# Optimization experiments

Measured on AMD Instinct MI355X. Metric: run time of the kernel, lower is better.

The kernel has to match this reference:

```python
import jax, jax.numpy as jnp
import numpy as np


def sign_fn(x):
    # torch.sign(torch.sign(x) + 0.5): maps x >= 0 -> +1, x < 0 -> -1 (zero -> +1)
    return jnp.where(x >= 0, 1.0, -1.0).astype(x.dtype)


def setup_inputs() -> dict:
    key = jax.random.key(0)
    kx, kw, kb = jax.random.split(key, 3)
    TOKENS, IN, OUT = 8192, 4096, 4096
    x = jax.random.normal(kx, (TOKENS, IN), dtype=jnp.float32)
    weight = jax.random.normal(kw, (OUT, IN), dtype=jnp.float32)
    bias = jax.random.normal(kb, (OUT,), dtype=jnp.float32)
    return {"x": x, "weight": weight, "bias": bias}


def reference(x, weight, bias):
    b_weight = sign_fn(weight)  # [out, in], values in {+1, -1}
    b_bias = sign_fn(bias)      # [out]
    # nn.functional.linear: y = x @ W^T + b
    return jnp.einsum('ti,oi->to', x, b_weight) + b_bias
```

## Files before the change

### kernel.cpp

```cpp
#include <hip/hip_runtime.h>


typedef __attribute__((ext_vector_type(4))) int   i32x4;
typedef __attribute__((ext_vector_type(8))) short short8;
typedef __attribute__((ext_vector_type(4))) float f32x4;

constexpr int M = 8192;
constexpr int N = 4096;
constexpr int K = 4096;

constexpr int BM = 256, BN = 256, BK = 64;
constexpr int NTILES = K / BK;
constexpr int TILE_A = BM * BK;
constexpr int TILE_B = BN * BK;
constexpr int BUFSZ  = TILE_A + TILE_B;
constexpr int RING   = 4;

__device__ __forceinline__ void load_lds16(const void* g, void* l) {
    __builtin_amdgcn_global_load_lds(
        (const __attribute__((address_space(1))) unsigned int*)g,
        (__attribute__((address_space(3))) unsigned int*)l, 16, 0, 0);
}

constexpr int XB = M / 4;
constexpr int WB = 1024;
constexpr int WCH = N * K / 8;

__global__ __launch_bounds__(256) void prep_fused(
    const float* __restrict__ X, const float* __restrict__ W,
    signed char* __restrict__ Xq, signed char* __restrict__ Wq,
    float* __restrict__ Scale) {
    const int t    = threadIdx.x;
    const int lane = t & 63;
    const int wv   = t >> 6;

    if (blockIdx.x < XB) {
        const int row = blockIdx.x * 4 + wv;
        const float4* xr = reinterpret_cast<const float4*>(X + (size_t)row * K);
        float4 v[16];
        float mx = 0.f;
#pragma unroll
        for (int i = 0; i < 4; ++i) {
#pragma unroll
            for (int j = 0; j < 4; ++j) {
                float4 f = xr[4 * lane + 256 * i + j];
                v[4 * i + j] = f;
                mx = fmaxf(mx, fmaxf(fmaxf(fabsf(f.x), fabsf(f.y)),
                                     fmaxf(fabsf(f.z), fabsf(f.w))));
            }
        }
#pragma unroll
        for (int off = 32; off > 0; off >>= 1)
            mx = fmaxf(mx, __shfl_down(mx, off));
        mx = __shfl(mx, 0);
        const float rmax = fmaxf(mx, 1e-20f);
        const float inv  = 127.f / rmax;
        if (lane == 0) Scale[row] = rmax * (1.f / 127.f);

        uint4* out4 = reinterpret_cast<uint4*>(Xq + (size_t)row * K);
#pragma unroll
        for (int i = 0; i < 4; ++i) {
            uint4 o;
            unsigned int* op = &o.x;
#pragma unroll
            for (int j = 0; j < 4; ++j) {
                float4 f = v[4 * i + j];
                int q0 = (int)rintf(f.x * inv);
                int q1 = (int)rintf(f.y * inv);
                int q2 = (int)rintf(f.z * inv);
                int q3 = (int)rintf(f.w * inv);
                op[j] = (q0 & 255) | ((q1 & 255) << 8) |
                        ((q2 & 255) << 16) | ((unsigned)(q3 & 255) << 24);
            }
            out4[lane + 64 * i] = o;
        }
    } else {
        const float4* W4 = reinterpret_cast<const float4*>(W);
        uint2* O = reinterpret_cast<uint2*>(Wq);
        auto sg = [](float f) -> unsigned int { return (f >= 0.f) ? 1u : 0xFFu; };
        size_t idx = (size_t)(blockIdx.x - XB) * 256 + t;
        const size_t stride = (size_t)WB * 256;
        for (size_t c = idx; c < (size_t)WCH; c += stride) {
            float4 a = W4[c * 2], b = W4[c * 2 + 1];
            uint2 o;
            o.x = sg(a.x) | (sg(a.y) << 8) | (sg(a.z) << 16) | (sg(a.w) << 24);
            o.y = sg(b.x) | (sg(b.y) << 8) | (sg(b.z) << 16) | (sg(b.w) << 24);
            O[c] = o;
        }
    }
}

struct GemmCtx {
    const signed char* gA0;
    const signed char* gA1;
    const signed char* gB0;
    const signed char* gB1;
    signed char* lbase;
    int wm, wn, rl, cq16;
};

template <bool STAGE, int VMEND>
__device__ __forceinline__ void kstep2(
    const GemmCtx& c, const signed char* smem, int t,
    i32x4 (&b)[4], i32x4 (&acc)[8][4]) {
    const signed char* Ab = smem + (t & (RING - 1)) * BUFSZ;
    const signed char* Bb = Ab + TILE_A;
    signed char* dst = c.lbase + ((t + 3) & (RING - 1)) * BUFSZ;
    const size_t ko = (size_t)(t + 3) * BK;

    if constexpr (VMEND >= 0)
        asm volatile("s_waitcnt vmcnt(%0)" :: "i"(VMEND) : "memory");
    __builtin_amdgcn_s_barrier();

    i32x4 a0[4];
#pragma unroll
    for (int ni = 0; ni < 4; ++ni)
        b[ni] = *reinterpret_cast<const i32x4*>(
            Bb + (c.wn * 64 + ni * 16 + c.rl) * BK + c.cq16);
#pragma unroll
    for (int mi = 0; mi < 4; ++mi)
        a0[mi] = *reinterpret_cast<const i32x4*>(
            Ab + (c.wm * 128 + mi * 16 + c.rl) * BK + c.cq16);
    if constexpr (STAGE) {
        load_lds16(c.gA0 + ko, dst);
        load_lds16(c.gA1 + ko, dst + 8192);
    }
    __builtin_amdgcn_s_setprio(1);
#pragma unroll
    for (int mi = 0; mi < 4; ++mi)
#pragma unroll
        for (int ni = 0; ni < 4; ++ni)
            acc[mi][ni] = __builtin_amdgcn_mfma_i32_16x16x64_i8(
                a0[mi], b[ni], acc[mi][ni], 0, 0, 0);
    __builtin_amdgcn_s_setprio(0);

    i32x4 a1[4];
#pragma unroll
    for (int mi = 0; mi < 4; ++mi)
        a1[mi] = *reinterpret_cast<const i32x4*>(
            Ab + (c.wm * 128 + (4 + mi) * 16 + c.rl) * BK + c.cq16);
    if constexpr (STAGE) {
        load_lds16(c.gB0 + ko, dst + TILE_A);
        load_lds16(c.gB1 + ko, dst + TILE_A + 8192);
    }
    asm volatile("" ::: "memory");
    __builtin_amdgcn_s_barrier();
    __builtin_amdgcn_s_setprio(1);
#pragma unroll
    for (int mi = 0; mi < 4; ++mi)
#pragma unroll
        for (int ni = 0; ni < 4; ++ni)
            acc[4 + mi][ni] = __builtin_amdgcn_mfma_i32_16x16x64_i8(
                a1[mi], b[ni], acc[4 + mi][ni], 0, 0, 0);
    __builtin_amdgcn_s_setprio(0);
    asm volatile("" ::: "memory");
}

__global__ __launch_bounds__(512, 2) void gemm_i8_p(
    const signed char* __restrict__ Aq, const signed char* __restrict__ Bq,
    const float* __restrict__ Scale, const float* __restrict__ Bias,
    float* __restrict__ OUT) {
    __shared__ signed char smem[RING * BUFSZ];

    const int tid  = threadIdx.x;
    const int lane = tid & 63;
    const int w    = tid >> 6;
    GemmCtx c;
    c.wm = w >> 2;
    c.wn = w & 3;
    c.rl = lane & 15;
    c.cq16 = (((lane >> 4) ^ ((c.rl >> 1) & 3)) << 4);

    const int wg  = blockIdx.x;
    const int lin = (wg & 7) * 64 + (wg >> 3);
    const int n0  = (lin & 15) * BN;
    const int m0  = (lin >> 4) * BM;

    const int srow = tid >> 2;
    const int cg   = ((tid & 3) ^ ((srow >> 1) & 3)) * 16;
    c.gA0 = Aq + (size_t)(m0 + srow)       * K + cg;
    c.gA1 = Aq + (size_t)(m0 + 128 + srow) * K + cg;
    c.gB0 = Bq + (size_t)(n0 + srow)       * K + cg;
    c.gB1 = Bq + (size_t)(n0 + 128 + srow) * K + cg;
    c.lbase = smem + w * 1024;

    auto stage_full = [&](int t) {
        signed char* d = c.lbase + (t & (RING - 1)) * BUFSZ;
        const size_t ko = (size_t)t * BK;
        load_lds16(c.gA0 + ko, d);
        load_lds16(c.gA1 + ko, d + 8192);
        load_lds16(c.gB0 + ko, d + TILE_A);
        load_lds16(c.gB1 + ko, d + TILE_A + 8192);
    };

    i32x4 acc[8][4];
#pragma unroll
    for (int mi = 0; mi < 8; ++mi)
#pragma unroll
        for (int ni = 0; ni < 4; ++ni)
            acc[mi][ni] = (i32x4){0, 0, 0, 0};
    i32x4 b[4];

    stage_full(0); stage_full(1); stage_full(2);

    int t = 0;
    for (; t < NTILES - 3; ++t)
        kstep2<true, 8>(c, smem, t, b, acc);
    kstep2<false, 8>(c, smem, t, b, acc); ++t;
    kstep2<false, 4>(c, smem, t, b, acc); ++t;
    kstep2<false, 0>(c, smem, t, b, acc);

#pragma unroll
    for (int ni = 0; ni < 4; ++ni) {
        const int gcol = n0 + c.wn * 64 + ni * 16 + c.rl;
        const float sb = (Bias[gcol] >= 0.f) ? 1.f : -1.f;
#pragma unroll
        for (int mi = 0; mi < 8; ++mi) {
            const int growb = m0 + c.wm * 128 + mi * 16 + (lane >> 4) * 4;
            const float4 sc = *reinterpret_cast<const float4*>(&Scale[growb]);
            OUT[(size_t)(growb + 0) * N + gcol] = (float)acc[mi][ni][0] * sc.x + sb;
            OUT[(size_t)(growb + 1) * N + gcol] = (float)acc[mi][ni][1] * sc.y + sb;
            OUT[(size_t)(growb + 2) * N + gcol] = (float)acc[mi][ni][2] * sc.z + sb;
            OUT[(size_t)(growb + 3) * N + gcol] = (float)acc[mi][ni][3] * sc.w + sb;
        }
    }
}

constexpr int MT   = 128;
constexpr int NTF  = 128;
constexpr int LDSS = 40;
constexpr int KTB  = 32;
__device__ __forceinline__ unsigned short f2b(float f) {
    unsigned int u = __builtin_bit_cast(unsigned int, f);
    u += 0x7FFFu + ((u >> 16) & 1u);
    return (unsigned short)(u >> 16);
}
__global__ __launch_bounds__(256) void binlin_fallback(
    const float* __restrict__ X, const float* __restrict__ W,
    const float* __restrict__ B, float* __restrict__ OUT) {
    __shared__ unsigned short As[MT][LDSS];
    __shared__ unsigned short Bs[NTF][LDSS];
    const int tid  = threadIdx.x;
    const int lane = tid & 63;
    const int wave = tid >> 6;
    const int wm   = wave >> 1;
    const int wn   = wave & 1;
    const int m0 = blockIdx.y * MT;
    const int n0 = blockIdx.x * NTF;
    const int rl = lane & 15;
    const int kq = (lane >> 4) * 8;
    f32x4 acc[4][4];
#pragma unroll
    for (int mi = 0; mi < 4; ++mi)
#pragma unroll
        for (int ni = 0; ni < 4; ++ni)
            acc[mi][ni] = (f32x4){0.f, 0.f, 0.f, 0.f};
    for (int k0 = 0; k0 < K; k0 += KTB) {
#pragma unroll
        for (int it = 0; it < 4; ++it) {
            int g = tid + it * 256, row = g >> 3, c4 = (g & 7) << 2;
            float4 v = *reinterpret_cast<const float4*>(&X[(size_t)(m0 + row) * K + k0 + c4]);
            ushort4 h;
            h.x = f2b(v.x); h.y = f2b(v.y); h.z = f2b(v.z); h.w = f2b(v.w);
            *reinterpret_cast<ushort4*>(&As[row][c4]) = h;
        }
#pragma unroll
        for (int it = 0; it < 4; ++it) {
            int g = tid + it * 256, row = g >> 3, c4 = (g & 7) << 2;
            float4 v = *reinterpret_cast<const float4*>(&W[(size_t)(n0 + row) * K + k0 + c4]);
            ushort4 h;
            h.x = (v.x >= 0.f) ? 0x3F80u : 0xBF80u;
            h.y = (v.y >= 0.f) ? 0x3F80u : 0xBF80u;
            h.z = (v.z >= 0.f) ? 0x3F80u : 0xBF80u;
            h.w = (v.w >= 0.f) ? 0x3F80u : 0xBF80u;
            *reinterpret_cast<ushort4*>(&Bs[row][c4]) = h;
        }
        __syncthreads();
        short8 a[4], b[4];
#pragma unroll
        for (int mi = 0; mi < 4; ++mi)
            a[mi] = *reinterpret_cast<const short8*>(&As[wm * 64 + mi * 16 + rl][kq]);
#pragma unroll
        for (int ni = 0; ni < 4; ++ni)
            b[ni] = *reinterpret_cast<const short8*>(&Bs[wn * 64 + ni * 16 + rl][kq]);
#pragma unroll
        for (int mi = 0; mi < 4; ++mi)
#pragma unroll
            for (int ni = 0; ni < 4; ++ni)
                acc[mi][ni] = __builtin_amdgcn_mfma_f32_16x16x32_bf16(
                    a[mi], b[ni], acc[mi][ni], 0, 0, 0);
        __syncthreads();
    }
#pragma unroll
    for (int ni = 0; ni < 4; ++ni) {
        int gcol = n0 + wn * 64 + ni * 16 + rl;
        float sb = (B[gcol] >= 0.f) ? 1.f : -1.f;
#pragma unroll
        for (int mi = 0; mi < 4; ++mi) {
            int growb = m0 + wm * 64 + mi * 16 + (lane >> 4) * 4;
#pragma unroll
            for (int r = 0; r < 4; ++r)
                OUT[(size_t)(growb + r) * N + gcol] = acc[mi][ni][r] + sb;
        }
    }
}

extern "C" void kernel_launch(void* const* d_in, const int* in_sizes, int n_in,
                              void* d_out, int out_size, void* d_ws, size_t ws_size,
                              hipStream_t stream) {
    const float* x  = (const float*)d_in[0];
    const float* w  = (const float*)d_in[1];
    const float* b  = (const float*)d_in[2];
    float* out      = (float*)d_out;

    const size_t need = (size_t)M * K + (size_t)N * K + (size_t)M * sizeof(float);
    if (ws_size >= need) {
        signed char* Xq = (signed char*)d_ws;
        signed char* Wq = Xq + (size_t)M * K;
        float* Scale    = (float*)(Wq + (size_t)N * K);

        prep_fused<<<dim3(XB + WB), dim3(256), 0, stream>>>(x, w, Xq, Wq, Scale);
        gemm_i8_p<<<dim3((M / BM) * (N / BN)), dim3(512), 0, stream>>>(
            Xq, Wq, Scale, b, out);
    } else {
        dim3 grid(N / NTF, M / MT);
        binlin_fallback<<<grid, dim3(256), 0, stream>>>(x, w, b, out);
    }
}
```

Measured before the change: 405.5 us.

## Switch GEMM to double-buffered LDS with one barrier per k-step, retune prep

The int8 GEMM drops its 4-deep LDS ring with split staging and vmcnt-based waits. In its place is a 2-buffer scheme: each k-step issues the full next-tile load up front, computes, then waits for vmcnt(0) and hits a barrier. Launch bounds go to 4 waves per EU and the accumulator b-fragments become local, with the aim of raising occupancy and simplifying the schedule. The X-quantization prep now uses one row per 256-thread block with an LDS max reduction instead of one row per wave. The shallower pipeline exposes more global-load latency per step, and the occupancy hint may cause register spills given the 32 accumulator vectors.

```diff
diff --git a/kernel.cpp b/kernel.cpp
--- a/kernel.cpp
+++ b/kernel.cpp
@@ -14,7 +14,7 @@
 constexpr int TILE_A = BM * BK;
 constexpr int TILE_B = BN * BK;
 constexpr int BUFSZ  = TILE_A + TILE_B;
-constexpr int RING   = 4;
+constexpr int RING   = 2;
 
 __device__ __forceinline__ void load_lds16(const void* g, void* l) {
     __builtin_amdgcn_global_load_lds(
@@ -22,63 +22,53 @@
         (__attribute__((address_space(3))) unsigned int*)l, 16, 0, 0);
 }
 
-constexpr int XB = M / 4;
-constexpr int WB = 1024;
+constexpr int WB  = 1024;
 constexpr int WCH = N * K / 8;
 
 __global__ __launch_bounds__(256) void prep_fused(
     const float* __restrict__ X, const float* __restrict__ W,
     signed char* __restrict__ Xq, signed char* __restrict__ Wq,
     float* __restrict__ Scale) {
-    const int t    = threadIdx.x;
-    const int lane = t & 63;
-    const int wv   = t >> 6;
-
-    if (blockIdx.x < XB) {
-        const int row = blockIdx.x * 4 + wv;
+    __shared__ float wmax[4];
+    const int t = threadIdx.x;
+
+    if (blockIdx.x < M) {
+        const int row = blockIdx.x;
         const float4* xr = reinterpret_cast<const float4*>(X + (size_t)row * K);
-        float4 v[16];
+        float4 v[4];
         float mx = 0.f;
 #pragma unroll
         for (int i = 0; i < 4; ++i) {
-#pragma unroll
-            for (int j = 0; j < 4; ++j) {
-                float4 f = xr[4 * lane + 256 * i + j];
-                v[4 * i + j] = f;
-                mx = fmaxf(mx, fmaxf(fmaxf(fabsf(f.x), fabsf(f.y)),
-                                     fmaxf(fabsf(f.z), fabsf(f.w))));
-            }
+            v[i] = xr[t + i * 256];
+            mx = fmaxf(mx, fmaxf(fmaxf(fabsf(v[i].x), fabsf(v[i].y)),
+                                 fmaxf(fabsf(v[i].z), fabsf(v[i].w))));
         }
 #pragma unroll
         for (int off = 32; off > 0; off >>= 1)
             mx = fmaxf(mx, __shfl_down(mx, off));
-        mx = __shfl(mx, 0);
-        const float rmax = fmaxf(mx, 1e-20f);
-        const float inv  = 127.f / rmax;
-        if (lane == 0) Scale[row] = rmax * (1.f / 127.f);
-
-        uint4* out4 = reinterpret_cast<uint4*>(Xq + (size_t)row * K);
+        if ((t & 63) == 0) wmax[t >> 6] = mx;
+        __syncthreads();
+        float rmax = fmaxf(fmaxf(wmax[0], wmax[1]), fmaxf(wmax[2], wmax[3]));
+        rmax = fmaxf(rmax, 1e-20f);
+        const float inv = 127.f / rmax;
+        if (t == 0) Scale[row] = rmax * (1.f / 127.f);
+
+        unsigned int* out = reinterpret_cast<unsigned int*>(Xq + (size_t)row * K);
 #pragma unroll
         for (int i = 0; i < 4; ++i) {
-            uint4 o;
-            unsigned int* op = &o.x;
-#pragma unroll
-            for (int j = 0; j < 4; ++j) {
-                float4 f = v[4 * i + j];
-                int q0 = (int)rintf(f.x * inv);
-                int q1 = (int)rintf(f.y * inv);
-                int q2 = (int)rintf(f.z * inv);
-                int q3 = (int)rintf(f.w * inv);
-                op[j] = (q0 & 255) | ((q1 & 255) << 8) |
-                        ((q2 & 255) << 16) | ((unsigned)(q3 & 255) << 24);
-            }
-            out4[lane + 64 * i] = o;
+            int q0 = (int)rintf(v[i].x * inv);
+            int q1 = (int)rintf(v[i].y * inv);
+            int q2 = (int)rintf(v[i].z * inv);
+            int q3 = (int)rintf(v[i].w * inv);
+            unsigned int p = (q0 & 255) | ((q1 & 255) << 8) |
+                             ((q2 & 255) << 16) | ((unsigned)(q3 & 255) << 24);
+            out[t + i * 256] = p;
         }
     } else {
         const float4* W4 = reinterpret_cast<const float4*>(W);
         uint2* O = reinterpret_cast<uint2*>(Wq);
         auto sg = [](float f) -> unsigned int { return (f >= 0.f) ? 1u : 0xFFu; };
-        size_t idx = (size_t)(blockIdx.x - XB) * 256 + t;
+        size_t idx = (size_t)(blockIdx.x - M) * 256 + t;
         const size_t stride = (size_t)WB * 256;
         for (size_t c = idx; c < (size_t)WCH; c += stride) {
             float4 a = W4[c * 2], b = W4[c * 2 + 1];
@@ -99,20 +89,23 @@
     int wm, wn, rl, cq16;
 };
 
-template <bool STAGE, int VMEND>
-__device__ __forceinline__ void kstep2(
+template <bool STAGE, bool SYNC>
+__device__ __forceinline__ void kstep(
     const GemmCtx& c, const signed char* smem, int t,
-    i32x4 (&b)[4], i32x4 (&acc)[8][4]) {
+    i32x4 (&acc)[8][4]) {
     const signed char* Ab = smem + (t & (RING - 1)) * BUFSZ;
     const signed char* Bb = Ab + TILE_A;
-    signed char* dst = c.lbase + ((t + 3) & (RING - 1)) * BUFSZ;
-    const size_t ko = (size_t)(t + 3) * BK;
-
-    if constexpr (VMEND >= 0)
-        asm volatile("s_waitcnt vmcnt(%0)" :: "i"(VMEND) : "memory");
-    __builtin_amdgcn_s_barrier();
-
-    i32x4 a0[4];
+
+    if constexpr (STAGE) {
+        signed char* dst = c.lbase + ((t + 1) & (RING - 1)) * BUFSZ;
+        const size_t ko = (size_t)(t + 1) * BK;
+        load_lds16(c.gA0 + ko, dst);
+        load_lds16(c.gA1 + ko, dst + 8192);
+        load_lds16(c.gB0 + ko, dst + TILE_A);
+        load_lds16(c.gB1 + ko, dst + TILE_A + 8192);
+    }
+
+    i32x4 b[4], a0[4], a1[4];
 #pragma unroll
     for (int ni = 0; ni < 4; ++ni)
         b[ni] = *reinterpret_cast<const i32x4*>(
@@ -121,10 +114,6 @@
     for (int mi = 0; mi < 4; ++mi)
         a0[mi] = *reinterpret_cast<const i32x4*>(
             Ab + (c.wm * 128 + mi * 16 + c.rl) * BK + c.cq16);
-    if constexpr (STAGE) {
-        load_lds16(c.gA0 + ko, dst);
-        load_lds16(c.gA1 + ko, dst + 8192);
-    }
     __builtin_amdgcn_s_setprio(1);
 #pragma unroll
     for (int mi = 0; mi < 4; ++mi)
@@ -133,18 +122,10 @@
             acc[mi][ni] = __builtin_amdgcn_mfma_i32_16x16x64_i8(
                 a0[mi], b[ni], acc[mi][ni], 0, 0, 0);
     __builtin_amdgcn_s_setprio(0);
-
-    i32x4 a1[4];
 #pragma unroll
     for (int mi = 0; mi < 4; ++mi)
         a1[mi] = *reinterpret_cast<const i32x4*>(
             Ab + (c.wm * 128 + (4 + mi) * 16 + c.rl) * BK + c.cq16);
-    if constexpr (STAGE) {
-        load_lds16(c.gB0 + ko, dst + TILE_A);
-        load_lds16(c.gB1 + ko, dst + TILE_A + 8192);
-    }
-    asm volatile("" ::: "memory");
-    __builtin_amdgcn_s_barrier();
     __builtin_amdgcn_s_setprio(1);
 #pragma unroll
     for (int mi = 0; mi < 4; ++mi)
@@ -153,10 +134,16 @@
             acc[4 + mi][ni] = __builtin_amdgcn_mfma_i32_16x16x64_i8(
                 a1[mi], b[ni], acc[4 + mi][ni], 0, 0, 0);
     __builtin_amdgcn_s_setprio(0);
-    asm volatile("" ::: "memory");
-}
-
-__global__ __launch_bounds__(512, 2) void gemm_i8_p(
+
+    if constexpr (SYNC) {
+        asm volatile("" ::: "memory");
+        asm volatile("s_waitcnt vmcnt(0)" ::: "memory");
+        __builtin_amdgcn_s_barrier();
+        asm volatile("" ::: "memory");
+    }
+}
+
+__global__ __launch_bounds__(512, 4) void gemm_i8_p(
     const signed char* __restrict__ Aq, const signed char* __restrict__ Bq,
     const float* __restrict__ Scale, const float* __restrict__ Bias,
     float* __restrict__ OUT) {
@@ -184,31 +171,27 @@
     c.gB1 = Bq + (size_t)(n0 + 128 + srow) * K + cg;
     c.lbase = smem + w * 1024;
 
-    auto stage_full = [&](int t) {
-        signed char* d = c.lbase + (t & (RING - 1)) * BUFSZ;
-        const size_t ko = (size_t)t * BK;
-        load_lds16(c.gA0 + ko, d);
-        load_lds16(c.gA1 + ko, d + 8192);
-        load_lds16(c.gB0 + ko, d + TILE_A);
-        load_lds16(c.gB1 + ko, d + TILE_A + 8192);
-    };
-
     i32x4 acc[8][4];
 #pragma unroll
     for (int mi = 0; mi < 8; ++mi)
 #pragma unroll
         for (int ni = 0; ni < 4; ++ni)
             acc[mi][ni] = (i32x4){0, 0, 0, 0};
-    i32x4 b[4];
-
-    stage_full(0); stage_full(1); stage_full(2);
-
-    int t = 0;
-    for (; t < NTILES - 3; ++t)
-        kstep2<true, 8>(c, smem, t, b, acc);
-    kstep2<false, 8>(c, smem, t, b, acc); ++t;
-    kstep2<false, 4>(c, smem, t, b, acc); ++t;
-    kstep2<false, 0>(c, smem, t, b, acc);
+
+    {
+        signed char* d = c.lbase;
+        load_lds16(c.gA0, d);
+        load_lds16(c.gA1, d + 8192);
+        load_lds16(c.gB0, d + TILE_A);
+        load_lds16(c.gB1, d + TILE_A + 8192);
+        asm volatile("s_waitcnt vmcnt(0)" ::: "memory");
+        __builtin_amdgcn_s_barrier();
+        asm volatile("" ::: "memory");
+    }
+
+    for (int t = 0; t < NTILES - 1; ++t)
+        kstep<true, true>(c, smem, t, acc);
+    kstep<false, false>(c, smem, NTILES - 1, acc);
 
 #pragma unroll
     for (int ni = 0; ni < 4; ++ni) {
@@ -319,7 +302,7 @@
         signed char* Wq = Xq + (size_t)M * K;
         float* Scale    = (float*)(Wq + (size_t)N * K);
 
-        prep_fused<<<dim3(XB + WB), dim3(256), 0, stream>>>(x, w, Xq, Wq, Scale);
+        prep_fused<<<dim3(M + WB), dim3(256), 0, stream>>>(x, w, Xq, Wq, Scale);
         gemm_i8_p<<<dim3((M / BM) * (N / BN)), dim3(512), 0, stream>>>(
             Xq, Wq, Scale, b, out);
     } else {
```

Result: slower. 1.246 ms (+207.4%).
